# Optimization experiments

Measured on AMD Instinct MI355X. Metric: run time of the kernel, lower is better.

## Reference

```python
import jax, jax.numpy as jnp
import numpy as np

HEAD_DIM = 128
L2_EPS = 1e-6


def l2norm(x):
    # RMS-style L2Norm: computed in fp32, cast back (matches L2Norm.forward)
    x32 = x.astype(jnp.float32)
    y = x32 * jax.lax.rsqrt(jnp.mean(x32 * x32, axis=-1, keepdims=True) + L2_EPS)
    return y.astype(x.dtype)


def setup_inputs() -> dict:
    key = jax.random.key(0)
    ks = jax.random.split(key, 8)
    B, S, D = 16, 1, 4096
    NKV, HD, MAXS = 8, HEAD_DIM, 4096
    w_scale = 0.02
    return {
        "x": jax.random.normal(ks[0], (B, S, D), dtype=jnp.float32),
        "wq": jax.random.normal(ks[1], (D, D), dtype=jnp.float32) * w_scale,
        "wk": jax.random.normal(ks[2], (D, NKV * HD), dtype=jnp.float32) * w_scale,
        "wv": jax.random.normal(ks[3], (D, NKV * HD), dtype=jnp.float32) * w_scale,
        "wo": jax.random.normal(ks[4], (D, D), dtype=jnp.float32) * w_scale,
        "cache_k": jax.random.normal(ks[5], (B, MAXS, NKV, HD), dtype=jnp.float32),
        "cache_v": jax.random.normal(ks[6], (B, MAXS, NKV, HD), dtype=jnp.float32),
        "freqs_complex": jax.random.normal(ks[7], (1, 64), dtype=jnp.float32),  # unused, as in source
        "start_pos": 4095,
    }


def reference(x, wq, wk, wv, wo, cache_k, cache_v, freqs_complex, start_pos):
    b, s, d = x.shape
    hd = HEAD_DIM
    n_kv = cache_k.shape[2]
    n_q = wq.shape[1] // hd
    n_rep = n_q // n_kv

    # QKV projections (Linear, no bias)
    xq = (x @ wq).reshape(b, s, n_q, hd)
    xk = (x @ wk).reshape(b, s, n_kv, hd)
    xv = (x @ wv).reshape(b, s, n_kv, hd)

    # qk_norm active since dim <= 4096
    xq = l2norm(xq)
    xk = l2norm(xk)

    # KV-cache append at start_pos (start_pos is a static Python int)
    cache_k = jax.lax.dynamic_update_slice(cache_k, xk, (0, start_pos, 0, 0))
    cache_v = jax.lax.dynamic_update_slice(cache_v, xv, (0, start_pos, 0, 0))
    keys = cache_k[:, : start_pos + s]    # [b, T, n_kv, hd]
    values = cache_v[:, : start_pos + s]  # [b, T, n_kv, hd]

    # GQA: group query heads as (n_kv, n_rep); equivalent to repeat_kv without
    # materializing the repeated KV tensors.
    xq = xq.reshape(b, s, n_kv, n_rep, hd)
    scores = jnp.einsum("bqgrd,bkgd->bgrqk", xq, keys) / np.float32(np.sqrt(hd))
    scores = jax.nn.softmax(scores.astype(jnp.float32), axis=-1).astype(xq.dtype)
    out = jnp.einsum("bgrqk,bkgd->bqgrd", scores, values).reshape(b, s, n_q * hd)
    return out @ wo
```

## Files before the change

kernel.cpp:

```cpp
#include <hip/hip_runtime.h>

#define D_MODEL 4096
#define NKV     8
#define NREP    4
#define HD      128
#define BATCH   16
#define SEQ     4096
#define NCOLS   6144
#define SPLITS  32
#define KC      128
#define NS      16
#define CHUNK   256

#define OFF_QKVP 0
#define OFF_ATTO 0
#define OFF_WOP  0
#define OFF_QKV  3145728
#define OFF_ATTM 3244032
#define OFF_ATTL 3252224
#define OFF_XO   3260416

__global__ __launch_bounds__(256) void qkv_partial(
    const float* __restrict__ x, const float* __restrict__ wq,
    const float* __restrict__ wk, const float* __restrict__ wv,
    float* __restrict__ part)
{
  __shared__ float xs[BATCH * KC];
  int tid = threadIdx.x;
  int sp  = blockIdx.y;
  int k0  = sp * KC;
  for (int i = tid; i < BATCH * KC; i += 256) {
    int b = i >> 7, kk = i & (KC - 1);
    xs[i] = x[(size_t)b * D_MODEL + k0 + kk];
  }
  __syncthreads();

  int w = tid >> 6, lane = tid & 63;
  int col = blockIdx.x * 512 + w * 128 + lane * 2;
  const float* wm; int c; int N;
  if (col < 4096)      { wm = wq; c = col;        N = 4096; }
  else if (col < 5120) { wm = wk; c = col - 4096; N = 1024; }
  else                 { wm = wv; c = col - 5120; N = 1024; }
  const float* wp = wm + (size_t)k0 * N + c;

  float accx[BATCH], accy[BATCH];
#pragma unroll
  for (int b = 0; b < BATCH; ++b) { accx[b] = 0.f; accy[b] = 0.f; }
#pragma unroll 2
  for (int kk = 0; kk < KC; kk += 8) {
    float2 wr[8];
#pragma unroll
    for (int j = 0; j < 8; ++j)
      wr[j] = *reinterpret_cast<const float2*>(wp + (size_t)(kk + j) * N);
#pragma unroll
    for (int b = 0; b < BATCH; ++b) {
      float4 xa = *reinterpret_cast<const float4*>(xs + b * KC + kk);
      float4 xb = *reinterpret_cast<const float4*>(xs + b * KC + kk + 4);
      float tx = accx[b], ty = accy[b];
      tx = fmaf(xa.x, wr[0].x, tx); ty = fmaf(xa.x, wr[0].y, ty);
      tx = fmaf(xa.y, wr[1].x, tx); ty = fmaf(xa.y, wr[1].y, ty);
      tx = fmaf(xa.z, wr[2].x, tx); ty = fmaf(xa.z, wr[2].y, ty);
      tx = fmaf(xa.w, wr[3].x, tx); ty = fmaf(xa.w, wr[3].y, ty);
      tx = fmaf(xb.x, wr[4].x, tx); ty = fmaf(xb.x, wr[4].y, ty);
      tx = fmaf(xb.y, wr[5].x, tx); ty = fmaf(xb.y, wr[5].y, ty);
      tx = fmaf(xb.z, wr[6].x, tx); ty = fmaf(xb.z, wr[6].y, ty);
      tx = fmaf(xb.w, wr[7].x, tx); ty = fmaf(xb.w, wr[7].y, ty);
      accx[b] = tx; accy[b] = ty;
    }
  }
#pragma unroll
  for (int b = 0; b < BATCH; ++b)
    *reinterpret_cast<float2*>(&part[(size_t)(sp * BATCH + b) * NCOLS + col]) =
        make_float2(accx[b], accy[b]);
}

__global__ __launch_bounds__(128) void qkv_finalize(
    const float* __restrict__ part, float* __restrict__ qkv)
{
  __shared__ float red[2];
  int blk = blockIdx.x;
  int b = blk / 48, h = blk - b * 48;
  int col = h * HD + threadIdx.x;
  float v = 0.f;
#pragma unroll
  for (int s = 0; s < SPLITS; ++s)
    v += part[(size_t)(s * BATCH + b) * NCOLS + col];
  float ss = v * v;
#pragma unroll
  for (int off = 32; off; off >>= 1) ss += __shfl_xor(ss, off);
  if ((threadIdx.x & 63) == 0) red[threadIdx.x >> 6] = ss;
  __syncthreads();
  float tot = red[0] + red[1];
  if (h < 40)
    v *= rsqrtf(tot * (1.f / 128.f) + 1e-6f);
  qkv[(size_t)b * NCOLS + col] = v;
}

__global__ __launch_bounds__(256, 4) void attn_partial(
    const float* __restrict__ cache_k, const float* __restrict__ cache_v,
    const float* __restrict__ qkv,
    float* __restrict__ attO, float* __restrict__ attM, float* __restrict__ attL)
{
  __shared__ float qs[NREP * HD];
  __shared__ float sc[NREP * CHUNK];
  __shared__ float op[4 * NREP * HD];
  int tid = threadIdx.x;
  int bg = blockIdx.x;
  int sp = blockIdx.y;
  int b = bg >> 3, g = bg & 7;

  const float* qsrc = qkv + (size_t)b * NCOLS + g * (NREP * HD);
  for (int i = tid; i < NREP * HD; i += 256) qs[i] = qsrc[i];
  __syncthreads();

  int pos0 = sp * CHUNK;
  const float* kbase  = cache_k + ((size_t)b * SEQ * NKV + g) * HD;
  const float* kfresh = qkv + (size_t)b * NCOLS + 4096 + g * HD;
  const float scl = 0.08838834764831845f;

  {
    int pl = tid >> 2, dq = tid & 3;
#pragma unroll 2
    for (int pass = 0; pass < 4; ++pass) {
      int pc  = pass * 64 + pl;
      int pos = pos0 + pc;
      const float* kv = (pos == SEQ - 1) ? kfresh
                                         : (kbase + (size_t)pos * (NKV * HD));
      float4 kr[8];
#pragma unroll
      for (int j = 0; j < 8; ++j)
        kr[j] = *reinterpret_cast<const float4*>(kv + j * 16 + dq * 4);
      float a[NREP];
#pragma unroll
      for (int r = 0; r < NREP; ++r) a[r] = 0.f;
#pragma unroll
      for (int j = 0; j < 8; ++j) {
#pragma unroll
        for (int r = 0; r < NREP; ++r) {
          float4 qv = *reinterpret_cast<const float4*>(qs + r * HD + j * 16 + dq * 4);
          a[r] += kr[j].x * qv.x + kr[j].y * qv.y + kr[j].z * qv.z + kr[j].w * qv.w;
        }
      }
#pragma unroll
      for (int r = 0; r < NREP; ++r) {
        a[r] += __shfl_xor(a[r], 1);
        a[r] += __shfl_xor(a[r], 2);
      }
      float out = (dq == 0) ? a[0] : (dq == 1) ? a[1] : (dq == 2) ? a[2] : a[3];
      sc[dq * CHUNK + pc] = out * scl;
    }
  }
  __syncthreads();

  int wv_ = tid >> 6, lane = tid & 63;
  float m_reg, l_reg;
  {
    float vals[4];
    float m = -1e30f;
#pragma unroll
    for (int i = 0; i < 4; ++i) { vals[i] = sc[wv_ * CHUNK + i * 64 + lane]; m = fmaxf(m, vals[i]); }
#pragma unroll
    for (int off = 32; off; off >>= 1) m = fmaxf(m, __shfl_xor(m, off));
    float l = 0.f;
#pragma unroll
    for (int i = 0; i < 4; ++i) { float p = __expf(vals[i] - m); sc[wv_ * CHUNK + i * 64 + lane] = p; l += p; }
#pragma unroll
    for (int off = 32; off; off >>= 1) l += __shfl_xor(l, off);
    m_reg = m; l_reg = l;
  }
  __syncthreads();

  {
    int quarter = wv_;
    int dl = lane * 2;
    const float* vbase  = cache_v + ((size_t)b * SEQ * NKV + g) * HD;
    const float* vfresh = qkv + (size_t)b * NCOLS + 5120 + g * HD;
    float a00=0,a01=0,a10=0,a11=0,a20=0,a21=0,a30=0,a31=0;
    int pb = pos0 + quarter * 64;
    for (int j = 0; j < 64; j += 8) {
#pragma unroll
      for (int u = 0; u < 8; ++u) {
        int pos = pb + j + u;
        const float* vp = (pos == SEQ - 1) ? vfresh : (vbase + (size_t)pos * (NKV * HD));
        float2 vd = *reinterpret_cast<const float2*>(vp + dl);
        int qp = quarter * 64 + j + u;
        float p0 = sc[0 * CHUNK + qp];
        float p1 = sc[1 * CHUNK + qp];
        float p2 = sc[2 * CHUNK + qp];
        float p3 = sc[3 * CHUNK + qp];
        a00 = fmaf(p0, vd.x, a00); a01 = fmaf(p0, vd.y, a01);
        a10 = fmaf(p1, vd.x, a10); a11 = fmaf(p1, vd.y, a11);
        a20 = fmaf(p2, vd.x, a20); a21 = fmaf(p2, vd.y, a21);
        a30 = fmaf(p3, vd.x, a30); a31 = fmaf(p3, vd.y, a31);
      }
    }
    *reinterpret_cast<float2*>(op + (quarter * NREP + 0) * HD + dl) = make_float2(a00, a01);
    *reinterpret_cast<float2*>(op + (quarter * NREP + 1) * HD + dl) = make_float2(a10, a11);
    *reinterpret_cast<float2*>(op + (quarter * NREP + 2) * HD + dl) = make_float2(a20, a21);
    *reinterpret_cast<float2*>(op + (quarter * NREP + 3) * HD + dl) = make_float2(a30, a31);
  }
  __syncthreads();

  size_t base = (size_t)(bg * NS + sp);
  for (int i = tid; i < NREP * HD; i += 256) {
    int r = i >> 7, d = i & 127;
    float o = op[(0*NREP + r)*HD + d] + op[(1*NREP + r)*HD + d]
            + op[(2*NREP + r)*HD + d] + op[(3*NREP + r)*HD + d];
    attO[base * (NREP * HD) + i] = o;
  }
  if (lane == 0) { attM[base * 4 + wv_] = m_reg; attL[base * 4 + wv_] = l_reg; }
}

__global__ __launch_bounds__(512) void attn_combine(
    const float* __restrict__ attO, const float* __restrict__ attM,
    const float* __restrict__ attL, float* __restrict__ xo)
{
  int bg = blockIdx.x;
  int tid = threadIdx.x;
  int r = tid >> 7;
  float m_s[NS];
  float M = -1e30f;
#pragma unroll
  for (int s = 0; s < NS; ++s) {
    m_s[s] = attM[(size_t)(bg * NS + s) * 4 + r];
    M = fmaxf(M, m_s[s]);
  }
  float L = 0.f, o = 0.f;
#pragma unroll
  for (int s = 0; s < NS; ++s) {
    float f = __expf(m_s[s] - M);
    L += attL[(size_t)(bg * NS + s) * 4 + r] * f;
    o += attO[(size_t)(bg * NS + s) * 512 + tid] * f;
  }
  int b = bg >> 3, g = bg & 7;
  xo[(size_t)b * D_MODEL + g * 512 + tid] = o / L;
}

__global__ __launch_bounds__(256) void wo_partial(
    const float* __restrict__ xo, const float* __restrict__ wo,
    float* __restrict__ part)
{
  __shared__ float xs[BATCH * KC];
  int tid = threadIdx.x;
  int sp  = blockIdx.y;
  int k0  = sp * KC;
  for (int i = tid; i < BATCH * KC; i += 256) {
    int b = i >> 7, kk = i & (KC - 1);
    xs[i] = xo[(size_t)b * D_MODEL + k0 + kk];
  }
  __syncthreads();

  int w = tid >> 6, lane = tid & 63;
  int col = blockIdx.x * 512 + w * 128 + lane * 2;
  const float* wp = wo + (size_t)k0 * D_MODEL + col;

  float accx[BATCH], accy[BATCH];
#pragma unroll
  for (int b = 0; b < BATCH; ++b) { accx[b] = 0.f; accy[b] = 0.f; }
#pragma unroll 2
  for (int kk = 0; kk < KC; kk += 8) {
    float2 wr[8];
#pragma unroll
    for (int j = 0; j < 8; ++j)
      wr[j] = *reinterpret_cast<const float2*>(wp + (size_t)(kk + j) * D_MODEL);
#pragma unroll
    for (int b = 0; b < BATCH; ++b) {
      float4 xa = *reinterpret_cast<const float4*>(xs + b * KC + kk);
      float4 xb = *reinterpret_cast<const float4*>(xs + b * KC + kk + 4);
      float tx = accx[b], ty = accy[b];
      tx = fmaf(xa.x, wr[0].x, tx); ty = fmaf(xa.x, wr[0].y, ty);
      tx = fmaf(xa.y, wr[1].x, tx); ty = fmaf(xa.y, wr[1].y, ty);
      tx = fmaf(xa.z, wr[2].x, tx); ty = fmaf(xa.z, wr[2].y, ty);
      tx = fmaf(xa.w, wr[3].x, tx); ty = fmaf(xa.w, wr[3].y, ty);
      tx = fmaf(xb.x, wr[4].x, tx); ty = fmaf(xb.x, wr[4].y, ty);
      tx = fmaf(xb.y, wr[5].x, tx); ty = fmaf(xb.y, wr[5].y, ty);
      tx = fmaf(xb.z, wr[6].x, tx); ty = fmaf(xb.z, wr[6].y, ty);
      tx = fmaf(xb.w, wr[7].x, tx); ty = fmaf(xb.w, wr[7].y, ty);
      accx[b] = tx; accy[b] = ty;
    }
  }
#pragma unroll
  for (int b = 0; b < BATCH; ++b)
    *reinterpret_cast<float2*>(&part[(size_t)(sp * BATCH + b) * D_MODEL + col]) =
        make_float2(accx[b], accy[b]);
}

__global__ __launch_bounds__(256) void wo_finalize(
    const float* __restrict__ part, float* __restrict__ out)
{
  int i = blockIdx.x * 256 + threadIdx.x;
  float v = 0.f;
#pragma unroll
  for (int s = 0; s < SPLITS; ++s)
    v += part[(size_t)s * (BATCH * D_MODEL) + i];
  out[i] = v;
}

extern "C" void kernel_launch(void* const* d_in, const int* in_sizes, int n_in,
                              void* d_out, int out_size, void* d_ws, size_t ws_size,
                              hipStream_t stream) {
  const float* x       = (const float*)d_in[0];
  const float* wq      = (const float*)d_in[1];
  const float* wk      = (const float*)d_in[2];
  const float* wv      = (const float*)d_in[3];
  const float* wo      = (const float*)d_in[4];
  const float* cache_k = (const float*)d_in[5];
  const float* cache_v = (const float*)d_in[6];
  float* out  = (float*)d_out;
  float* wsf  = (float*)d_ws;
  float* qkvp = wsf + OFF_QKVP;
  float* qkv  = wsf + OFF_QKV;
  float* attO = wsf + OFF_ATTO;
  float* attM = wsf + OFF_ATTM;
  float* attL = wsf + OFF_ATTL;
  float* xo   = wsf + OFF_XO;
  float* wop  = wsf + OFF_WOP;

  qkv_partial <<<dim3(12, 32), 256, 0, stream>>>(x, wq, wk, wv, qkvp);
  qkv_finalize<<<BATCH * 48, 128, 0, stream>>>(qkvp, qkv);
  attn_partial<<<dim3(BATCH * NKV, NS), 256, 0, stream>>>(cache_k, cache_v, qkv, attO, attM, attL);
  attn_combine<<<BATCH * NKV, 512, 0, stream>>>(attO, attM, attL, xo);
  wo_partial  <<<dim3(8, 32), 256, 0, stream>>>(xo, wo, wop);
  wo_finalize <<<256, 256, 0, stream>>>(wop, out);
}
```

Baseline: 691.1 us.

## Restructure attention partial to process all KV groups per block with contiguous rows

Each attention block now covers one batch and a 128-position chunk across all 8 KV heads, with 512 threads, so every K/V row read spans a full contiguous 4 KB line instead of a strided 512-byte slice per head. The split count doubles to 32, and each wave handles one KV group over the whole chunk, which removes the cross-wave shared-memory reduction of partial outputs. Shared-memory arrays are padded to avoid bank conflicts. The grid shrinks to 512 blocks of twice the size, which changes occupancy and adds more partials for the combine step to merge.

```diff
diff --git a/kernel.cpp b/kernel.cpp
--- a/kernel.cpp
+++ b/kernel.cpp
@@ -9,16 +9,18 @@
 #define NCOLS   6144
 #define SPLITS  32
 #define KC      128
-#define NS      16
-#define CHUNK   256
+#define NS      32
+#define CHUNK   128
+#define SD      129
+#define QSTR    516
 
 #define OFF_QKVP 0
 #define OFF_ATTO 0
 #define OFF_WOP  0
 #define OFF_QKV  3145728
 #define OFF_ATTM 3244032
-#define OFF_ATTL 3252224
-#define OFF_XO   3260416
+#define OFF_ATTL 3260416
+#define OFF_XO   3276800
 
 __global__ __launch_bounds__(256) void qkv_partial(
     const float* __restrict__ x, const float* __restrict__ wq,
@@ -96,48 +98,53 @@
   qkv[(size_t)b * NCOLS + col] = v;
 }
 
-__global__ __launch_bounds__(256, 4) void attn_partial(
+__global__ __launch_bounds__(512, 4) void attn_partial(
     const float* __restrict__ cache_k, const float* __restrict__ cache_v,
     const float* __restrict__ qkv,
     float* __restrict__ attO, float* __restrict__ attM, float* __restrict__ attL)
 {
-  __shared__ float qs[NREP * HD];
-  __shared__ float sc[NREP * CHUNK];
-  __shared__ float op[4 * NREP * HD];
+  __shared__ float qs[NKV * QSTR];
+  __shared__ float sc[NKV * NREP * SD];
   int tid = threadIdx.x;
-  int bg = blockIdx.x;
-  int sp = blockIdx.y;
-  int b = bg >> 3, g = bg & 7;
-
-  const float* qsrc = qkv + (size_t)b * NCOLS + g * (NREP * HD);
-  for (int i = tid; i < NREP * HD; i += 256) qs[i] = qsrc[i];
-  __syncthreads();
-
+  int b   = blockIdx.x;
+  int sp  = blockIdx.y;
   int pos0 = sp * CHUNK;
-  const float* kbase  = cache_k + ((size_t)b * SEQ * NKV + g) * HD;
-  const float* kfresh = qkv + (size_t)b * NCOLS + 4096 + g * HD;
+
+  {
+    const float* qsrc = qkv + (size_t)b * NCOLS;
+    for (int idx = tid; idx < NKV * NREP * HD / 4; idx += 512) {
+      int g = idx >> 7, i4 = (idx & 127) * 4;
+      *reinterpret_cast<float4*>(qs + g * QSTR + i4) =
+          *reinterpret_cast<const float4*>(qsrc + g * 512 + i4);
+    }
+  }
+  __syncthreads();
+
   const float scl = 0.08838834764831845f;
 
   {
-    int pl = tid >> 2, dq = tid & 3;
-#pragma unroll 2
-    for (int pass = 0; pass < 4; ++pass) {
-      int pc  = pass * 64 + pl;
-      int pos = pos0 + pc;
+    int dq = tid & 3;
+    int gid = tid >> 2;
+    int g  = gid & 7;
+    int pr = gid >> 3;
+    const float* qg = qs + g * QSTR;
+    const float* kfresh = qkv + (size_t)b * NCOLS + 4096 + g * HD;
+#pragma unroll 1
+    for (int pass = 0; pass < 8; ++pass) {
+      int posc = pass * 16 + pr;
+      int pos  = pos0 + posc;
       const float* kv = (pos == SEQ - 1) ? kfresh
-                                         : (kbase + (size_t)pos * (NKV * HD));
+          : (cache_k + ((size_t)b * SEQ + pos) * (NKV * HD) + g * HD);
       float4 kr[8];
 #pragma unroll
       for (int j = 0; j < 8; ++j)
         kr[j] = *reinterpret_cast<const float4*>(kv + j * 16 + dq * 4);
-      float a[NREP];
-#pragma unroll
-      for (int r = 0; r < NREP; ++r) a[r] = 0.f;
+      float a[NREP] = {0.f, 0.f, 0.f, 0.f};
 #pragma unroll
       for (int j = 0; j < 8; ++j) {
 #pragma unroll
         for (int r = 0; r < NREP; ++r) {
-          float4 qv = *reinterpret_cast<const float4*>(qs + r * HD + j * 16 + dq * 4);
+          float4 qv = *reinterpret_cast<const float4*>(qg + r * HD + j * 16 + dq * 4);
           a[r] += kr[j].x * qv.x + kr[j].y * qv.y + kr[j].z * qv.z + kr[j].w * qv.w;
         }
       }
@@ -146,69 +153,65 @@
         a[r] += __shfl_xor(a[r], 1);
         a[r] += __shfl_xor(a[r], 2);
       }
-      float out = (dq == 0) ? a[0] : (dq == 1) ? a[1] : (dq == 2) ? a[2] : a[3];
-      sc[dq * CHUNK + pc] = out * scl;
-    }
-  }
-  __syncthreads();
-
-  int wv_ = tid >> 6, lane = tid & 63;
-  float m_reg, l_reg;
+      float v = (dq == 0) ? a[0] : (dq == 1) ? a[1] : (dq == 2) ? a[2] : a[3];
+      sc[(g * 4 + dq) * SD + posc] = v * scl;
+    }
+  }
+  __syncthreads();
+
+  int g = tid >> 6, lane = tid & 63;
   {
-    float vals[4];
-    float m = -1e30f;
-#pragma unroll
-    for (int i = 0; i < 4; ++i) { vals[i] = sc[wv_ * CHUNK + i * 64 + lane]; m = fmaxf(m, vals[i]); }
-#pragma unroll
-    for (int off = 32; off; off >>= 1) m = fmaxf(m, __shfl_xor(m, off));
-    float l = 0.f;
-#pragma unroll
-    for (int i = 0; i < 4; ++i) { float p = __expf(vals[i] - m); sc[wv_ * CHUNK + i * 64 + lane] = p; l += p; }
-#pragma unroll
-    for (int off = 32; off; off >>= 1) l += __shfl_xor(l, off);
-    m_reg = m; l_reg = l;
+#pragma unroll
+    for (int r = 0; r < NREP; ++r) {
+      float v0 = sc[(g * 4 + r) * SD + lane];
+      float v1 = sc[(g * 4 + r) * SD + 64 + lane];
+      float m = fmaxf(v0, v1);
+#pragma unroll
+      for (int off = 32; off; off >>= 1) m = fmaxf(m, __shfl_xor(m, off));
+      float p0 = __expf(v0 - m), p1 = __expf(v1 - m);
+      sc[(g * 4 + r) * SD + lane]      = p0;
+      sc[(g * 4 + r) * SD + 64 + lane] = p1;
+      float l = p0 + p1;
+#pragma unroll
+      for (int off = 32; off; off >>= 1) l += __shfl_xor(l, off);
+      if (lane == 0) {
+        size_t mi = (((size_t)b * NKV + g) * NS + sp) * 4 + r;
+        attM[mi] = m;
+        attL[mi] = l;
+      }
+    }
   }
   __syncthreads();
 
   {
-    int quarter = wv_;
     int dl = lane * 2;
-    const float* vbase  = cache_v + ((size_t)b * SEQ * NKV + g) * HD;
     const float* vfresh = qkv + (size_t)b * NCOLS + 5120 + g * HD;
-    float a00=0,a01=0,a10=0,a11=0,a20=0,a21=0,a30=0,a31=0;
-    int pb = pos0 + quarter * 64;
-    for (int j = 0; j < 64; j += 8) {
+    const float* vb = cache_v + (size_t)b * SEQ * (NKV * HD) + g * HD;
+    const float* pr_ = sc + g * 4 * SD;
+    float ax0=0,ay0=0,ax1=0,ay1=0,ax2=0,ay2=0,ax3=0,ay3=0;
+    for (int j = 0; j < CHUNK; j += 8) {
 #pragma unroll
       for (int u = 0; u < 8; ++u) {
-        int pos = pb + j + u;
-        const float* vp = (pos == SEQ - 1) ? vfresh : (vbase + (size_t)pos * (NKV * HD));
+        int posc = j + u;
+        int pos = pos0 + posc;
+        const float* vp = (pos == SEQ - 1) ? vfresh : (vb + (size_t)pos * (NKV * HD));
         float2 vd = *reinterpret_cast<const float2*>(vp + dl);
-        int qp = quarter * 64 + j + u;
-        float p0 = sc[0 * CHUNK + qp];
-        float p1 = sc[1 * CHUNK + qp];
-        float p2 = sc[2 * CHUNK + qp];
-        float p3 = sc[3 * CHUNK + qp];
-        a00 = fmaf(p0, vd.x, a00); a01 = fmaf(p0, vd.y, a01);
-        a10 = fmaf(p1, vd.x, a10); a11 = fmaf(p1, vd.y, a11);
-        a20 = fmaf(p2, vd.x, a20); a21 = fmaf(p2, vd.y, a21);
-        a30 = fmaf(p3, vd.x, a30); a31 = fmaf(p3, vd.y, a31);
+        float p0 = pr_[0 * SD + posc];
+        float p1 = pr_[1 * SD + posc];
+        float p2 = pr_[2 * SD + posc];
+        float p3 = pr_[3 * SD + posc];
+        ax0 = fmaf(p0, vd.x, ax0); ay0 = fmaf(p0, vd.y, ay0);
+        ax1 = fmaf(p1, vd.x, ax1); ay1 = fmaf(p1, vd.y, ay1);
+        ax2 = fmaf(p2, vd.x, ax2); ay2 = fmaf(p2, vd.y, ay2);
+        ax3 = fmaf(p3, vd.x, ax3); ay3 = fmaf(p3, vd.y, ay3);
       }
     }
-    *reinterpret_cast<float2*>(op + (quarter * NREP + 0) * HD + dl) = make_float2(a00, a01);
-    *reinterpret_cast<float2*>(op + (quarter * NREP + 1) * HD + dl) = make_float2(a10, a11);
-    *reinterpret_cast<float2*>(op + (quarter * NREP + 2) * HD + dl) = make_float2(a20, a21);
-    *reinterpret_cast<float2*>(op + (quarter * NREP + 3) * HD + dl) = make_float2(a30, a31);
-  }
-  __syncthreads();
-
-  size_t base = (size_t)(bg * NS + sp);
-  for (int i = tid; i < NREP * HD; i += 256) {
-    int r = i >> 7, d = i & 127;
-    float o = op[(0*NREP + r)*HD + d] + op[(1*NREP + r)*HD + d]
-            + op[(2*NREP + r)*HD + d] + op[(3*NREP + r)*HD + d];
-    attO[base * (NREP * HD) + i] = o;
-  }
-  if (lane == 0) { attM[base * 4 + wv_] = m_reg; attL[base * 4 + wv_] = l_reg; }
+    size_t ob = (((size_t)b * NKV + g) * NS + sp) * (NREP * HD);
+    *reinterpret_cast<float2*>(attO + ob + 0 * HD + dl) = make_float2(ax0, ay0);
+    *reinterpret_cast<float2*>(attO + ob + 1 * HD + dl) = make_float2(ax1, ay1);
+    *reinterpret_cast<float2*>(attO + ob + 2 * HD + dl) = make_float2(ax2, ay2);
+    *reinterpret_cast<float2*>(attO + ob + 3 * HD + dl) = make_float2(ax3, ay3);
+  }
 }
 
 __global__ __launch_bounds__(512) void attn_combine(
@@ -318,7 +321,7 @@
 
   qkv_partial <<<dim3(12, 32), 256, 0, stream>>>(x, wq, wk, wv, qkvp);
   qkv_finalize<<<BATCH * 48, 128, 0, stream>>>(qkvp, qkv);
-  attn_partial<<<dim3(BATCH * NKV, NS), 256, 0, stream>>>(cache_k, cache_v, qkv, attO, attM, attL);
+  attn_partial<<<dim3(BATCH, NS), 512, 0, stream>>>(cache_k, cache_v, qkv, attO, attM, attL);
   attn_combine<<<BATCH * NKV, 512, 0, stream>>>(attO, attM, attL, xo);
   wo_partial  <<<dim3(8, 32), 256, 0, stream>>>(xo, wo, wop);
   wo_finalize <<<256, 256, 0, stream>>>(wop, out);
```

After: 688.2 us. Within noise of the previous version (-0.4%).
